# Optimization experiments

Hardware: AMD Instinct MI355X
Metric: run time of the kernel (lower is better)

## Reference

```python
import jax, jax.numpy as jnp
import numpy as np

HEADS = 4
DIM_HEAD = 32
SCALE = DIM_HEAD ** -0.5
EPS = 1e-5


def setup_inputs() -> dict:
    key = jax.random.key(0)
    k1, k2, k3, k4 = jax.random.split(key, 4)
    dim = 256
    hidden = HEADS * DIM_HEAD  # 128
    x = jax.random.normal(k1, (16, dim, 64, 64), dtype=jnp.float32)
    # 1x1 conv weights stored as [out_ch, in_ch] (kernel size 1 squeezed)
    w_qkv = jax.random.normal(k2, (hidden * 3, dim), dtype=jnp.float32) * (dim ** -0.5)
    w_out = jax.random.normal(k3, (dim, hidden), dtype=jnp.float32) * (hidden ** -0.5)
    b_out = jax.random.normal(k4, (dim,), dtype=jnp.float32) * 0.01
    g = jnp.ones((1, dim, 1, 1), dtype=jnp.float32)  # LayerNorm gain
    return {"x": x, "w_qkv": w_qkv, "w_out": w_out, "b_out": b_out, "g": g}


def reference(x, w_qkv, w_out, b_out, g):
    b, c, h, w = x.shape
    n = h * w
    # 1x1 conv to qkv: [b, 3*hidden, h, w]
    qkv = jnp.einsum('oc,bchw->bohw', w_qkv, x)
    q, k, v = jnp.split(qkv, 3, axis=1)

    def to_heads(t):
        return t.reshape(b, HEADS, DIM_HEAD, n)  # b h d n

    q, k, v = to_heads(q), to_heads(k), to_heads(v)
    q = jax.nn.softmax(q, axis=2) * SCALE       # softmax over head-dim d
    k = jax.nn.softmax(k, axis=3)               # softmax over spatial n
    v = v / n                                    # v / (h*w)
    context = jnp.einsum('bhdn,bhen->bhde', k, v)
    out = jnp.einsum('bhde,bhdn->bhen', context, q)  # b h e n
    out = out.reshape(b, HEADS * DIM_HEAD, h, w)
    # output 1x1 conv with bias
    out = jnp.einsum('oc,bchw->bohw', w_out, out) + b_out[None, :, None, None]
    # channel LayerNorm (biased variance over dim=1)
    mean = jnp.mean(out, axis=1, keepdims=True)
    var = jnp.var(out, axis=1, keepdims=True)
    return (out - mean) * jax.lax.rsqrt(var + EPS) * g
```

## Files before the change

### kernel.cpp

```cpp
#include <hip/hip_runtime.h>

typedef short short8 __attribute__((ext_vector_type(8)));
typedef float f32x16 __attribute__((ext_vector_type(16)));
typedef unsigned short ushort_t;

#define B_    16
#define C_    256
#define N_    4096
#define H_    4
#define HID_  128
#define SCALE_ 0.17677669529663687f
#define EPS_  1e-5f

__device__ inline ushort_t f2bf(float f) {
  union { float f; unsigned u; } a; a.f = f;
  unsigned r = a.u + 0x7FFFu + ((a.u >> 16) & 1u);
  return (ushort_t)(r >> 16);
}

__device__ inline int2 pack4(float a, float b, float c, float d) {
  int2 o;
  o.x = (int)f2bf(a) | ((int)f2bf(b) << 16);
  o.y = (int)f2bf(c) | ((int)f2bf(d) << 16);
  return o;
}

__device__ inline short8 ld_frag16(const ushort_t* p) {
  return __builtin_bit_cast(short8, *(const int4*)p);
}
__device__ inline short8 ld_frag8(const ushort_t* p) {
  int2 a = *(const int2*)p, b = *(const int2*)(p + 4);
  int4 t; t.x = a.x; t.y = a.y; t.z = b.x; t.w = b.y;
  return __builtin_bit_cast(short8, t);
}

__global__ void k0_wswz(const float* __restrict__ w, ushort_t* __restrict__ wsw) {
  int gid = blockIdx.x * 256 + threadIdx.x;
  int ln = gid & 63, kc = (gid >> 6) & 15, mt = gid >> 10;
  int row = mt * 32 + (ln & 31);
  int col = kc * 16 + (ln >> 5) * 8;
  const float* src = w + (size_t)row * 256 + col;
  float4 a = *(const float4*)src, b = *(const float4*)(src + 4);
  union { ushort_t u[8]; int4 v; } o;
  o.u[0] = f2bf(a.x); o.u[1] = f2bf(a.y); o.u[2] = f2bf(a.z); o.u[3] = f2bf(a.w);
  o.u[4] = f2bf(b.x); o.u[5] = f2bf(b.y); o.u[6] = f2bf(b.z); o.u[7] = f2bf(b.w);
  *(int4*)(wsw + (size_t)gid * 8) = o.v;
}

__global__ __launch_bounds__(512, 4) void k1_qkv(
    const float* __restrict__ x, const ushort_t* __restrict__ wsw,
    ushort_t* __restrict__ qp, float* __restrict__ pctx, float* __restrict__ psum)
{
  __shared__ __align__(16) union {
    ushort_t Xs[64 * 264];
    struct { ushort_t kt[128 * 68]; ushort_t vt[128 * 68]; } s2;
  } sm;

  const int tid = threadIdx.x;
  const int b = blockIdx.y;
  const int blk = blockIdx.x;
  const int n0 = blk * 64;
  const int w = tid >> 6, lane = tid & 63;
  const int half = lane >> 5, lm = lane & 31;
  const int hw = w >> 1, ntile = w & 1;
  const int gnt = blk * 2 + ntile;

  {
    const float* xsrc = x + (size_t)b * C_ * N_ + n0;
    const int n4 = tid & 15;
    const int cqA = tid >> 4;
    const int cqB = cqA + 32;
    const float* pA = xsrc + (size_t)(cqA * 4) * N_ + n4 * 4;
    const float* pB = xsrc + (size_t)(cqB * 4) * N_ + n4 * 4;
    float4 a0 = *(const float4*)(pA);
    float4 a1 = *(const float4*)(pA + N_);
    float4 a2 = *(const float4*)(pA + 2 * N_);
    float4 a3 = *(const float4*)(pA + 3 * N_);
    float4 b0 = *(const float4*)(pB);
    float4 b1 = *(const float4*)(pB + N_);
    float4 b2 = *(const float4*)(pB + 2 * N_);
    float4 b3 = *(const float4*)(pB + 3 * N_);
    ushort_t* dA = sm.Xs + (((cqA >> 1) ^ n4) * 8 + (cqA & 1) * 4) + (n4 * 4) * 264;
    ushort_t* dB = sm.Xs + (((cqB >> 1) ^ n4) * 8 + (cqB & 1) * 4) + (n4 * 4) * 264;
    *(int2*)(dA + 0 * 264) = pack4(a0.x, a1.x, a2.x, a3.x);
    *(int2*)(dA + 1 * 264) = pack4(a0.y, a1.y, a2.y, a3.y);
    *(int2*)(dA + 2 * 264) = pack4(a0.z, a1.z, a2.z, a3.z);
    *(int2*)(dA + 3 * 264) = pack4(a0.w, a1.w, a2.w, a3.w);
    *(int2*)(dB + 0 * 264) = pack4(b0.x, b1.x, b2.x, b3.x);
    *(int2*)(dB + 1 * 264) = pack4(b0.y, b1.y, b2.y, b3.y);
    *(int2*)(dB + 2 * 264) = pack4(b0.z, b1.z, b2.z, b3.z);
    *(int2*)(dB + 3 * 264) = pack4(b0.w, b1.w, b2.w, b3.w);
  }
  __syncthreads();

  f32x16 acc0, acc1, acc2;
  for (int r = 0; r < 16; ++r) { acc0[r] = 0.0f; acc1[r] = 0.0f; acc2[r] = 0.0f; }
  {
    const ushort_t* xrow = sm.Xs + (ntile * 32 + lm) * 264;
    const int sn = ntile * 8 + (lm >> 2);
    for (int kc = 0; kc < 16; ++kc) {
      short8 bfrag = ld_frag16(xrow + (((2 * kc + half) ^ sn) << 3));
      short8 af0 = ld_frag16(wsw + (size_t)(((hw) * 16 + kc) * 64 + lane) * 8);
      short8 af1 = ld_frag16(wsw + (size_t)(((4 + hw) * 16 + kc) * 64 + lane) * 8);
      short8 af2 = ld_frag16(wsw + (size_t)(((8 + hw) * 16 + kc) * 64 + lane) * 8);
      acc0 = __builtin_amdgcn_mfma_f32_32x32x16_bf16(af0, bfrag, acc0, 0, 0, 0);
      acc1 = __builtin_amdgcn_mfma_f32_32x32x16_bf16(af1, bfrag, acc1, 0, 0, 0);
      acc2 = __builtin_amdgcn_mfma_f32_32x32x16_bf16(af2, bfrag, acc2, 0, 0, 0);
    }
  }

  {
    float m = -1e30f;
    for (int r = 0; r < 16; ++r) m = fmaxf(m, acc0[r]);
    m = fmaxf(m, __shfl_xor(m, 32));
    float qe[16];
    float s = 0.0f;
    for (int r = 0; r < 16; ++r) { qe[r] = __expf(acc0[r] - m); s += qe[r]; }
    s += __shfl_xor(s, 32);
    float sc = SCALE_ / s;
    ushort_t* qpb = qp + (size_t)b * N_ * 128;
    for (int q = 0; q < 4; ++q) {
      int kc = hw * 2 + (q >> 1);
      int fl = (q & 1) * 32 + lm;
      int2 o = pack4(qe[q * 4 + 0] * sc, qe[q * 4 + 1] * sc,
                     qe[q * 4 + 2] * sc, qe[q * 4 + 3] * sc);
      *(int2*)(qpb + (size_t)((gnt * 8 + kc) * 64 + fl) * 8 + 4 * half) = o;
    }
  }

  float ev[16];
  for (int r = 0; r < 16; ++r) ev[r] = __expf(acc1[r]);

  __syncthreads();

  for (int r = 0; r < 16; ++r) {
    int row = (r & 3) + 8 * (r >> 2) + 4 * half;
    sm.s2.kt[(hw * 32 + row) * 68 + ntile * 32 + lm] = f2bf(ev[r]);
    sm.s2.vt[(hw * 32 + row) * 68 + ntile * 32 + lm] = f2bf(acc2[r]);
  }

  for (int mask = 1; mask <= 16; mask <<= 1)
    for (int r = 0; r < 16; ++r) ev[r] += __shfl_xor(ev[r], mask);
  if (lm == 0) {
    float* ps = psum + ((size_t)(b * 4 + hw) * 128 + gnt) * 32;
    for (int r = 0; r < 16; ++r) {
      int row = (r & 3) + 8 * (r >> 2) + 4 * half;
      ps[row] = ev[r];
    }
  }
  __syncthreads();

  if (ntile == 0) {
    f32x16 cacc;
    for (int r = 0; r < 16; ++r) cacc[r] = 0.0f;
    const ushort_t* ka = sm.s2.kt + (hw * 32 + lm) * 68 + half * 8;
    const ushort_t* va = sm.s2.vt + (hw * 32 + lm) * 68 + half * 8;
    for (int s = 0; s < 4; ++s) {
      short8 af = ld_frag8(ka + s * 16);
      short8 bf = ld_frag8(va + s * 16);
      cacc = __builtin_amdgcn_mfma_f32_32x32x16_bf16(af, bf, cacc, 0, 0, 0);
    }
    float* pc = pctx + ((size_t)(b * 4 + hw) * 64 + blk) * 1024;
    for (int r = 0; r < 16; ++r) {
      int row = (r & 3) + 8 * (r >> 2) + 4 * half;
      pc[row * 32 + lm] = cacc[r];
    }
  }
}

__global__ __launch_bounds__(256) void kr_reduce(
    const float* __restrict__ pctx, const float* __restrict__ psum,
    float* __restrict__ ctxr, float* __restrict__ psumr)
{
  __shared__ float red[8][32];
  const int tid = threadIdx.x;
  const int q = blockIdx.x;
  const int bh = blockIdx.y;
  const int idx = q * 256 + tid;
  const float* src = pctx + (size_t)bh * 65536 + idx;
  float s = 0.0f;
  #pragma unroll 8
  for (int blk = 0; blk < 64; ++blk) s += src[blk * 1024];
  ctxr[(size_t)bh * 1024 + idx] = s;
  if (q == 0) {
    const int d = tid & 31, part = tid >> 5;
    const float* ps = psum + (size_t)bh * 4096 + part * 512 + d;
    float t = 0.0f;
    #pragma unroll
    for (int g = 0; g < 16; ++g) t += ps[g * 32];
    red[part][d] = t;
    __syncthreads();
    if (tid < 32) {
      float u = 0.0f;
      #pragma unroll
      for (int p = 0; p < 8; ++p) u += red[p][tid];
      psumr[(size_t)bh * 32 + tid] = u;
    }
  }
}

__global__ __launch_bounds__(256) void k2b_weff(
    const float* __restrict__ ctxr, const float* __restrict__ psumr,
    const float* __restrict__ wout, ushort_t* __restrict__ weff)
{
  __shared__ float ctxs[32][32];
  __shared__ float inv[32];
  const int tid = threadIdx.x;
  const int ph = blockIdx.x, pb = blockIdx.y;
  const size_t bh = (size_t)(pb * 4 + ph);
  float4 v = *(const float4*)(ctxr + bh * 1024 + tid * 4);
  if (tid < 32) inv[tid] = 1.0f / (psumr[bh * 32 + tid] * 4096.0f);
  __syncthreads();
  {
    float iv = inv[tid >> 3];
    float* crow = &ctxs[0][0] + tid * 4;
    crow[0] = v.x * iv; crow[1] = v.y * iv; crow[2] = v.z * iv; crow[3] = v.w * iv;
  }
  __syncthreads();
  {
    const int oc = tid;
    const int mt = oc >> 5, lmm = oc & 31;
    const float* wrow = wout + (size_t)oc * HID_ + ph * 32;
    float wr[32];
    for (int e = 0; e < 32; ++e) wr[e] = wrow[e];
    float vals[32];
    for (int d = 0; d < 32; ++d) {
      float s = 0.0f;
      for (int e = 0; e < 32; ++e) s += wr[e] * ctxs[d][e];
      vals[d] = s;
    }
    ushort_t* wb_b = weff + (size_t)pb * 32768;
    for (int kci = 0; kci < 2; ++kci) {
      int kc = ph * 2 + kci;
      for (int hf = 0; hf < 2; ++hf) {
        int d0 = kci * 16 + hf * 8;
        union { ushort_t u[8]; int4 v; } o;
        for (int j = 0; j < 8; ++j) o.u[j] = f2bf(vals[d0 + j]);
        *(int4*)(wb_b + (size_t)((mt * 8 + kc) * 64 + hf * 32 + lmm) * 8) = o.v;
      }
    }
  }
}

__global__ __launch_bounds__(256, 4) void k3_out(
    const ushort_t* __restrict__ weff, const ushort_t* __restrict__ qp,
    const float* __restrict__ bout, const float* __restrict__ g,
    float* __restrict__ out)
{
  __shared__ float part_s[2][64], part_s2[2][64];
  __shared__ float st_mu[64], st_rs[64];

  const int tid = threadIdx.x;
  const int b = blockIdx.y;
  const int blk = blockIdx.x;
  const int n0 = blk * 64;
  const int w = tid >> 6, lane = tid & 63;
  const int half = lane >> 5, lm = lane & 31;
  const int ntile = w & 1, mgrp = w >> 1;
  const int gnt = blk * 2 + ntile;

  f32x16 acc[4];
  for (int i = 0; i < 4; ++i)
    for (int r = 0; r < 16; ++r) acc[i][r] = 0.0f;

  {
    const ushort_t* qb = qp + (size_t)b * N_ * 128 + (size_t)gnt * 8 * 64 * 8;
    const ushort_t* wbase = weff + (size_t)b * 32768 + ((size_t)(mgrp * 4) * 8 * 64 + lane) * 8;
    for (int kc = 0; kc < 8; ++kc) {
      short8 bfrag = ld_frag16(qb + (size_t)(kc * 64 + lane) * 8);
      for (int i = 0; i < 4; ++i) {
        short8 af = ld_frag16(wbase + (size_t)((i * 8 + kc) * 64) * 8);
        acc[i] = __builtin_amdgcn_mfma_f32_32x32x16_bf16(af, bfrag, acc[i], 0, 0, 0);
      }
    }
  }

  float s = 0.0f, s2v = 0.0f;
  for (int i = 0; i < 4; ++i) {
    int mt = mgrp * 4 + i;
    for (int r = 0; r < 16; ++r) {
      int row = mt * 32 + (r & 3) + 8 * (r >> 2) + 4 * half;
      acc[i][r] += bout[row];
      float v = acc[i][r];
      s += v; s2v += v * v;
    }
  }
  s += __shfl_xor(s, 32);
  s2v += __shfl_xor(s2v, 32);
  if (half == 0) { part_s[mgrp][ntile * 32 + lm] = s; part_s2[mgrp][ntile * 32 + lm] = s2v; }
  __syncthreads();
  if (tid < 64) {
    float S = part_s[0][tid] + part_s[1][tid];
    float S2 = part_s2[0][tid] + part_s2[1][tid];
    float mu = S * (1.0f / 256.0f);
    float var = S2 * (1.0f / 256.0f) - mu * mu;
    st_mu[tid] = mu;
    st_rs[tid] = rsqrtf(var + EPS_);
  }
  __syncthreads();

  const int col = ntile * 32 + lm;
  const float mu = st_mu[col];
  const float rs = st_rs[col];
  float* ob = out + (size_t)b * C_ * N_ + n0 + col;
  for (int i = 0; i < 4; ++i) {
    int mt = mgrp * 4 + i;
    for (int r = 0; r < 16; ++r) {
      int row = mt * 32 + (r & 3) + 8 * (r >> 2) + 4 * half;
      ob[(size_t)row * N_] = (acc[i][r] - mu) * rs * g[row];
    }
  }
}

extern "C" void kernel_launch(void* const* d_in, const int* in_sizes, int n_in,
                              void* d_out, int out_size, void* d_ws, size_t ws_size,
                              hipStream_t stream) {
  (void)in_sizes; (void)n_in; (void)out_size; (void)ws_size;
  const float* x    = (const float*)d_in[0];
  const float* wqkv = (const float*)d_in[1];
  const float* wout = (const float*)d_in[2];
  const float* bout = (const float*)d_in[3];
  const float* g    = (const float*)d_in[4];
  float* out = (float*)d_out;

  char* ws = (char*)d_ws;
  ushort_t* qp    = (ushort_t*)(ws);
  float*    pctx  = (float*)(ws + ((size_t)16 << 20));
  float*    psum  = (float*)(ws + ((size_t)32 << 20));
  ushort_t* weff  = (ushort_t*)(ws + ((size_t)33 << 20));
  ushort_t* wsw   = (ushort_t*)(ws + ((size_t)34 << 20));
  float*    ctxr  = (float*)(ws + ((size_t)34 << 20) + (192 << 10));
  float*    psumr = (float*)(ws + ((size_t)34 << 20) + (448 << 10));

  k0_wswz<<<48, 256, 0, stream>>>(wqkv, wsw);
  k1_qkv<<<dim3(64, 16), 512, 0, stream>>>(x, wsw, qp, pctx, psum);
  kr_reduce<<<dim3(4, 64), 256, 0, stream>>>(pctx, psum, ctxr, psumr);
  k2b_weff<<<dim3(4, 16), 256, 0, stream>>>(ctxr, psumr, wout, weff);
  k3_out<<<dim3(64, 16), 256, 0, stream>>>(weff, qp, bout, g, out);
}
```

Measured before the change: 165.9 us.

## Halve qkv block size, compute k-sums via MFMA, fuse reduce with weff kernel

The qkv kernel now runs 256 threads per block, with each wave covering both 32-column n-tiles. This reuses each weight fragment across two MFMAs, and all four waves now do the context MFMA. The per-row exp(k) sums are computed with an MFMA against a ones vector instead of shuffle reductions. The separate reduce kernel is merged into the weff kernel, removing one launch and the intermediate buffers. The cost is more accumulator registers per thread, and a reduction phase in the merged kernel that runs only 64 blocks.

```diff
diff --git a/kernel.cpp b/kernel.cpp
--- a/kernel.cpp
+++ b/kernel.cpp
@@ -47,7 +47,7 @@
   *(int4*)(wsw + (size_t)gid * 8) = o.v;
 }
 
-__global__ __launch_bounds__(512, 4) void k1_qkv(
+__global__ __launch_bounds__(256, 3) void k1_qkv(
     const float* __restrict__ x, const ushort_t* __restrict__ wsw,
     ushort_t* __restrict__ qp, float* __restrict__ pctx, float* __restrict__ psum)
 {
@@ -60,161 +60,178 @@
   const int b = blockIdx.y;
   const int blk = blockIdx.x;
   const int n0 = blk * 64;
-  const int w = tid >> 6, lane = tid & 63;
+  const int hw = tid >> 6, lane = tid & 63;
   const int half = lane >> 5, lm = lane & 31;
-  const int hw = w >> 1, ntile = w & 1;
-  const int gnt = blk * 2 + ntile;
 
   {
     const float* xsrc = x + (size_t)b * C_ * N_ + n0;
     const int n4 = tid & 15;
-    const int cqA = tid >> 4;
-    const int cqB = cqA + 32;
-    const float* pA = xsrc + (size_t)(cqA * 4) * N_ + n4 * 4;
-    const float* pB = xsrc + (size_t)(cqB * 4) * N_ + n4 * 4;
-    float4 a0 = *(const float4*)(pA);
-    float4 a1 = *(const float4*)(pA + N_);
-    float4 a2 = *(const float4*)(pA + 2 * N_);
-    float4 a3 = *(const float4*)(pA + 3 * N_);
-    float4 b0 = *(const float4*)(pB);
-    float4 b1 = *(const float4*)(pB + N_);
-    float4 b2 = *(const float4*)(pB + 2 * N_);
-    float4 b3 = *(const float4*)(pB + 3 * N_);
-    ushort_t* dA = sm.Xs + (((cqA >> 1) ^ n4) * 8 + (cqA & 1) * 4) + (n4 * 4) * 264;
-    ushort_t* dB = sm.Xs + (((cqB >> 1) ^ n4) * 8 + (cqB & 1) * 4) + (n4 * 4) * 264;
-    *(int2*)(dA + 0 * 264) = pack4(a0.x, a1.x, a2.x, a3.x);
-    *(int2*)(dA + 1 * 264) = pack4(a0.y, a1.y, a2.y, a3.y);
-    *(int2*)(dA + 2 * 264) = pack4(a0.z, a1.z, a2.z, a3.z);
-    *(int2*)(dA + 3 * 264) = pack4(a0.w, a1.w, a2.w, a3.w);
-    *(int2*)(dB + 0 * 264) = pack4(b0.x, b1.x, b2.x, b3.x);
-    *(int2*)(dB + 1 * 264) = pack4(b0.y, b1.y, b2.y, b3.y);
-    *(int2*)(dB + 2 * 264) = pack4(b0.z, b1.z, b2.z, b3.z);
-    *(int2*)(dB + 3 * 264) = pack4(b0.w, b1.w, b2.w, b3.w);
-  }
-  __syncthreads();
-
-  f32x16 acc0, acc1, acc2;
-  for (int r = 0; r < 16; ++r) { acc0[r] = 0.0f; acc1[r] = 0.0f; acc2[r] = 0.0f; }
-  {
-    const ushort_t* xrow = sm.Xs + (ntile * 32 + lm) * 264;
-    const int sn = ntile * 8 + (lm >> 2);
+    const int cq0 = tid >> 4;
+    #pragma unroll
+    for (int cc = 0; cc < 4; ++cc) {
+      const int cq = cq0 + cc * 16;
+      const float* p = xsrc + (size_t)(cq * 4) * N_ + n4 * 4;
+      float4 a0 = *(const float4*)(p);
+      float4 a1 = *(const float4*)(p + N_);
+      float4 a2 = *(const float4*)(p + 2 * N_);
+      float4 a3 = *(const float4*)(p + 3 * N_);
+      ushort_t* d = sm.Xs + (((cq >> 1) ^ n4) * 8 + (cq & 1) * 4) + (n4 * 4) * 264;
+      *(int2*)(d + 0 * 264) = pack4(a0.x, a1.x, a2.x, a3.x);
+      *(int2*)(d + 1 * 264) = pack4(a0.y, a1.y, a2.y, a3.y);
+      *(int2*)(d + 2 * 264) = pack4(a0.z, a1.z, a2.z, a3.z);
+      *(int2*)(d + 3 * 264) = pack4(a0.w, a1.w, a2.w, a3.w);
+    }
+  }
+  __syncthreads();
+
+  f32x16 acc0a, acc0b, acc1a, acc1b, acc2a, acc2b;
+  for (int r = 0; r < 16; ++r) {
+    acc0a[r] = 0.0f; acc0b[r] = 0.0f; acc1a[r] = 0.0f;
+    acc1b[r] = 0.0f; acc2a[r] = 0.0f; acc2b[r] = 0.0f;
+  }
+  {
+    const ushort_t* xrow0 = sm.Xs + lm * 264;
+    const ushort_t* xrow1 = sm.Xs + (32 + lm) * 264;
+    const int sn0 = lm >> 2;
+    const int sn1 = 8 + (lm >> 2);
+    const ushort_t* wl = wsw + (size_t)(hw * 16 * 64 + lane) * 8;
+    #pragma unroll
     for (int kc = 0; kc < 16; ++kc) {
-      short8 bfrag = ld_frag16(xrow + (((2 * kc + half) ^ sn) << 3));
-      short8 af0 = ld_frag16(wsw + (size_t)(((hw) * 16 + kc) * 64 + lane) * 8);
-      short8 af1 = ld_frag16(wsw + (size_t)(((4 + hw) * 16 + kc) * 64 + lane) * 8);
-      short8 af2 = ld_frag16(wsw + (size_t)(((8 + hw) * 16 + kc) * 64 + lane) * 8);
-      acc0 = __builtin_amdgcn_mfma_f32_32x32x16_bf16(af0, bfrag, acc0, 0, 0, 0);
-      acc1 = __builtin_amdgcn_mfma_f32_32x32x16_bf16(af1, bfrag, acc1, 0, 0, 0);
-      acc2 = __builtin_amdgcn_mfma_f32_32x32x16_bf16(af2, bfrag, acc2, 0, 0, 0);
-    }
-  }
-
-  {
-    float m = -1e30f;
-    for (int r = 0; r < 16; ++r) m = fmaxf(m, acc0[r]);
-    m = fmaxf(m, __shfl_xor(m, 32));
-    float qe[16];
-    float s = 0.0f;
-    for (int r = 0; r < 16; ++r) { qe[r] = __expf(acc0[r] - m); s += qe[r]; }
-    s += __shfl_xor(s, 32);
-    float sc = SCALE_ / s;
+      short8 b0 = ld_frag16(xrow0 + (((2 * kc + half) ^ sn0) << 3));
+      short8 b1 = ld_frag16(xrow1 + (((2 * kc + half) ^ sn1) << 3));
+      short8 af0 = ld_frag16(wl + kc * 512);
+      short8 af1 = ld_frag16(wl + 32768 + kc * 512);
+      short8 af2 = ld_frag16(wl + 65536 + kc * 512);
+      acc0a = __builtin_amdgcn_mfma_f32_32x32x16_bf16(af0, b0, acc0a, 0, 0, 0);
+      acc0b = __builtin_amdgcn_mfma_f32_32x32x16_bf16(af0, b1, acc0b, 0, 0, 0);
+      acc1a = __builtin_amdgcn_mfma_f32_32x32x16_bf16(af1, b0, acc1a, 0, 0, 0);
+      acc1b = __builtin_amdgcn_mfma_f32_32x32x16_bf16(af1, b1, acc1b, 0, 0, 0);
+      acc2a = __builtin_amdgcn_mfma_f32_32x32x16_bf16(af2, b0, acc2a, 0, 0, 0);
+      acc2b = __builtin_amdgcn_mfma_f32_32x32x16_bf16(af2, b1, acc2b, 0, 0, 0);
+    }
+  }
+
+  {
     ushort_t* qpb = qp + (size_t)b * N_ * 128;
-    for (int q = 0; q < 4; ++q) {
-      int kc = hw * 2 + (q >> 1);
-      int fl = (q & 1) * 32 + lm;
-      int2 o = pack4(qe[q * 4 + 0] * sc, qe[q * 4 + 1] * sc,
-                     qe[q * 4 + 2] * sc, qe[q * 4 + 3] * sc);
-      *(int2*)(qpb + (size_t)((gnt * 8 + kc) * 64 + fl) * 8 + 4 * half) = o;
-    }
-  }
-
-  float ev[16];
-  for (int r = 0; r < 16; ++r) ev[r] = __expf(acc1[r]);
+    {
+      float m = -1e30f;
+      for (int r = 0; r < 16; ++r) m = fmaxf(m, acc0a[r]);
+      m = fmaxf(m, __shfl_xor(m, 32));
+      float qe[16]; float s = 0.0f;
+      for (int r = 0; r < 16; ++r) { qe[r] = __expf(acc0a[r] - m); s += qe[r]; }
+      s += __shfl_xor(s, 32);
+      float sc = SCALE_ / s;
+      const int gnt = blk * 2;
+      for (int q = 0; q < 4; ++q) {
+        int kc = hw * 2 + (q >> 1);
+        int fl = (q & 1) * 32 + lm;
+        int2 o = pack4(qe[q * 4 + 0] * sc, qe[q * 4 + 1] * sc,
+                       qe[q * 4 + 2] * sc, qe[q * 4 + 3] * sc);
+        *(int2*)(qpb + (size_t)((gnt * 8 + kc) * 64 + fl) * 8 + 4 * half) = o;
+      }
+    }
+    {
+      float m = -1e30f;
+      for (int r = 0; r < 16; ++r) m = fmaxf(m, acc0b[r]);
+      m = fmaxf(m, __shfl_xor(m, 32));
+      float qe[16]; float s = 0.0f;
+      for (int r = 0; r < 16; ++r) { qe[r] = __expf(acc0b[r] - m); s += qe[r]; }
+      s += __shfl_xor(s, 32);
+      float sc = SCALE_ / s;
+      const int gnt = blk * 2 + 1;
+      for (int q = 0; q < 4; ++q) {
+        int kc = hw * 2 + (q >> 1);
+        int fl = (q & 1) * 32 + lm;
+        int2 o = pack4(qe[q * 4 + 0] * sc, qe[q * 4 + 1] * sc,
+                       qe[q * 4 + 2] * sc, qe[q * 4 + 3] * sc);
+        *(int2*)(qpb + (size_t)((gnt * 8 + kc) * 64 + fl) * 8 + 4 * half) = o;
+      }
+    }
+  }
 
   __syncthreads();
 
   for (int r = 0; r < 16; ++r) {
     int row = (r & 3) + 8 * (r >> 2) + 4 * half;
-    sm.s2.kt[(hw * 32 + row) * 68 + ntile * 32 + lm] = f2bf(ev[r]);
-    sm.s2.vt[(hw * 32 + row) * 68 + ntile * 32 + lm] = f2bf(acc2[r]);
-  }
-
-  for (int mask = 1; mask <= 16; mask <<= 1)
-    for (int r = 0; r < 16; ++r) ev[r] += __shfl_xor(ev[r], mask);
-  if (lm == 0) {
-    float* ps = psum + ((size_t)(b * 4 + hw) * 128 + gnt) * 32;
-    for (int r = 0; r < 16; ++r) {
-      int row = (r & 3) + 8 * (r >> 2) + 4 * half;
-      ps[row] = ev[r];
-    }
-  }
-  __syncthreads();
-
-  if (ntile == 0) {
-    f32x16 cacc;
-    for (int r = 0; r < 16; ++r) cacc[r] = 0.0f;
+    ushort_t* krow = sm.s2.kt + (hw * 32 + row) * 68;
+    ushort_t* vrow = sm.s2.vt + (hw * 32 + row) * 68;
+    krow[lm]      = f2bf(__expf(acc1a[r]));
+    krow[32 + lm] = f2bf(__expf(acc1b[r]));
+    vrow[lm]      = f2bf(acc2a[r]);
+    vrow[32 + lm] = f2bf(acc2b[r]);
+  }
+  __syncthreads();
+
+  {
+    f32x16 cacc, sacc;
+    for (int r = 0; r < 16; ++r) { cacc[r] = 0.0f; sacc[r] = 0.0f; }
+    short8 ones;
+    #pragma unroll
+    for (int j = 0; j < 8; ++j) ones[j] = (short)0x3F80;
     const ushort_t* ka = sm.s2.kt + (hw * 32 + lm) * 68 + half * 8;
     const ushort_t* va = sm.s2.vt + (hw * 32 + lm) * 68 + half * 8;
-    for (int s = 0; s < 4; ++s) {
-      short8 af = ld_frag8(ka + s * 16);
-      short8 bf = ld_frag8(va + s * 16);
+    #pragma unroll
+    for (int ks = 0; ks < 4; ++ks) {
+      short8 af = ld_frag8(ka + ks * 16);
+      short8 bf = ld_frag8(va + ks * 16);
       cacc = __builtin_amdgcn_mfma_f32_32x32x16_bf16(af, bf, cacc, 0, 0, 0);
+      sacc = __builtin_amdgcn_mfma_f32_32x32x16_bf16(af, ones, sacc, 0, 0, 0);
     }
     float* pc = pctx + ((size_t)(b * 4 + hw) * 64 + blk) * 1024;
     for (int r = 0; r < 16; ++r) {
       int row = (r & 3) + 8 * (r >> 2) + 4 * half;
       pc[row * 32 + lm] = cacc[r];
     }
-  }
-}
-
-__global__ __launch_bounds__(256) void kr_reduce(
+    if (lm == 0) {
+      float* ps = psum + ((size_t)(b * 4 + hw) * 64 + blk) * 32;
+      for (int r = 0; r < 16; ++r) {
+        int row = (r & 3) + 8 * (r >> 2) + 4 * half;
+        ps[row] = sacc[r];
+      }
+    }
+  }
+}
+
+__global__ __launch_bounds__(256) void krw(
     const float* __restrict__ pctx, const float* __restrict__ psum,
-    float* __restrict__ ctxr, float* __restrict__ psumr)
-{
-  __shared__ float red[8][32];
-  const int tid = threadIdx.x;
-  const int q = blockIdx.x;
-  const int bh = blockIdx.y;
-  const int idx = q * 256 + tid;
-  const float* src = pctx + (size_t)bh * 65536 + idx;
-  float s = 0.0f;
-  #pragma unroll 8
-  for (int blk = 0; blk < 64; ++blk) s += src[blk * 1024];
-  ctxr[(size_t)bh * 1024 + idx] = s;
-  if (q == 0) {
-    const int d = tid & 31, part = tid >> 5;
-    const float* ps = psum + (size_t)bh * 4096 + part * 512 + d;
-    float t = 0.0f;
-    #pragma unroll
-    for (int g = 0; g < 16; ++g) t += ps[g * 32];
-    red[part][d] = t;
-    __syncthreads();
-    if (tid < 32) {
-      float u = 0.0f;
-      #pragma unroll
-      for (int p = 0; p < 8; ++p) u += red[p][tid];
-      psumr[(size_t)bh * 32 + tid] = u;
-    }
-  }
-}
-
-__global__ __launch_bounds__(256) void k2b_weff(
-    const float* __restrict__ ctxr, const float* __restrict__ psumr,
     const float* __restrict__ wout, ushort_t* __restrict__ weff)
 {
   __shared__ float ctxs[32][32];
   __shared__ float inv[32];
+  __shared__ float red[8][32];
   const int tid = threadIdx.x;
-  const int ph = blockIdx.x, pb = blockIdx.y;
-  const size_t bh = (size_t)(pb * 4 + ph);
-  float4 v = *(const float4*)(ctxr + bh * 1024 + tid * 4);
-  if (tid < 32) inv[tid] = 1.0f / (psumr[bh * 32 + tid] * 4096.0f);
+  const int bh = blockIdx.x;
+  const int pb = bh >> 2, ph = bh & 3;
+
+  {
+    const int d = tid & 31, part = tid >> 5;
+    const float* ps = psum + (size_t)bh * 2048 + part * 8 * 32 + d;
+    float t = 0.0f;
+    #pragma unroll
+    for (int g = 0; g < 8; ++g) t += ps[g * 32];
+    red[part][d] = t;
+  }
+  float4 s4 = make_float4(0.f, 0.f, 0.f, 0.f);
+  {
+    const float* pc = pctx + (size_t)bh * 65536 + tid * 4;
+    #pragma unroll 8
+    for (int c = 0; c < 64; ++c) {
+      float4 v = *(const float4*)(pc + c * 1024);
+      s4.x += v.x; s4.y += v.y; s4.z += v.z; s4.w += v.w;
+    }
+  }
+  __syncthreads();
+  if (tid < 32) {
+    float u = 0.0f;
+    #pragma unroll
+    for (int p = 0; p < 8; ++p) u += red[p][tid];
+    inv[tid] = 1.0f / (u * 4096.0f);
+  }
   __syncthreads();
   {
     float iv = inv[tid >> 3];
     float* crow = &ctxs[0][0] + tid * 4;
-    crow[0] = v.x * iv; crow[1] = v.y * iv; crow[2] = v.z * iv; crow[3] = v.w * iv;
+    crow[0] = s4.x * iv; crow[1] = s4.y * iv; crow[2] = s4.z * iv; crow[3] = s4.w * iv;
   }
   __syncthreads();
   {
@@ -327,14 +344,11 @@
   ushort_t* qp    = (ushort_t*)(ws);
   float*    pctx  = (float*)(ws + ((size_t)16 << 20));
   float*    psum  = (float*)(ws + ((size_t)32 << 20));
-  ushort_t* weff  = (ushort_t*)(ws + ((size_t)33 << 20));
-  ushort_t* wsw   = (ushort_t*)(ws + ((size_t)34 << 20));
-  float*    ctxr  = (float*)(ws + ((size_t)34 << 20) + (192 << 10));
-  float*    psumr = (float*)(ws + ((size_t)34 << 20) + (448 << 10));
+  ushort_t* weff  = (ushort_t*)(ws + ((size_t)32 << 20) + (512 << 10));
+  ushort_t* wsw   = (ushort_t*)(ws + ((size_t)33 << 20) + (512 << 10));
 
   k0_wswz<<<48, 256, 0, stream>>>(wqkv, wsw);
-  k1_qkv<<<dim3(64, 16), 512, 0, stream>>>(x, wsw, qp, pctx, psum);
-  kr_reduce<<<dim3(4, 64), 256, 0, stream>>>(pctx, psum, ctxr, psumr);
-  k2b_weff<<<dim3(4, 16), 256, 0, stream>>>(ctxr, psumr, wout, weff);
+  k1_qkv<<<dim3(64, 16), 256, 0, stream>>>(x, wsw, qp, pctx, psum);
+  krw<<<64, 256, 0, stream>>>(pctx, psum, wout, weff);
   k3_out<<<dim3(64, 16), 256, 0, stream>>>(weff, qp, bout, g, out);
 }
```

Measured after the change: 159.9 us. 1.04x faster.
